# Optimization experiments

Hardware: AMD Instinct MI355X
Metric: run time of the kernel (lower is better)

## Reference

```python
import jax, jax.numpy as jnp
import numpy as np
from jax import lax

B, T, D, H, L = 128, 512, 256, 256, 2


def setup_inputs() -> dict:
    key = jax.random.key(0)
    ks = jax.random.split(key, 8)
    s = 1.0 / np.sqrt(H)
    return {
        "input1": jax.random.normal(ks[0], (B, T, D), jnp.float32),
        "input2": jax.random.normal(ks[1], (B, T, D), jnp.float32),
        "W_ih": jax.random.normal(ks[2], (L, 4 * H, D), jnp.float32) * s,
        "W_hh": jax.random.normal(ks[3], (L, 4 * H, H), jnp.float32) * s,
        "b_ih": jax.random.normal(ks[4], (L, 4 * H), jnp.float32) * s,
        "b_hh": jax.random.normal(ks[5], (L, 4 * H), jnp.float32) * s,
        "fc_w": jax.random.normal(ks[6], (5, H), jnp.float32) * s,
        "fc_b": jax.random.normal(ks[7], (5,), jnp.float32) * s,
    }


def _lstm_layer(x, Wih, Whh, bih, bhh):
    # x: [B, T, in]; returns (outputs [B, T, H], final h [B, H])
    b = x.shape[0]
    # precompute input projection for all timesteps (one big GEMM)
    xg = jnp.einsum('bti,gi->btg', x, Wih) + bih + bhh  # [B, T, 4H]
    h0 = jnp.zeros((b, H), x.dtype)
    c0 = jnp.zeros((b, H), x.dtype)

    def step(carry, xg_t):
        h, c = carry
        gates = xg_t + h @ Whh.T  # [B, 4H]
        i, f, g, o = jnp.split(gates, 4, axis=-1)
        i = jax.nn.sigmoid(i)
        f = jax.nn.sigmoid(f)
        g = jnp.tanh(g)
        o = jax.nn.sigmoid(o)
        c = f * c + i * g
        h = o * jnp.tanh(c)
        return (h, c), h

    (h_last, _), hs = lax.scan(step, (h0, c0), jnp.swapaxes(xg, 0, 1))
    return jnp.swapaxes(hs, 0, 1), h_last


def _forward_once(x, W_ih, W_hh, b_ih, b_hh, fc_w, fc_b):
    h_finals = []
    out = x
    for l in range(L):
        out, h_last = _lstm_layer(out, W_ih[l], W_hh[l], b_ih[l], b_hh[l])
        h_finals.append(h_last)
    hn = jnp.stack(h_finals, axis=0).reshape(-1, H)  # [L*B, H] (torch hn.view)
    return jax.nn.relu(hn) @ fc_w.T + fc_b  # [L*B, 5]


def reference(input1, input2, W_ih, W_hh, b_ih, b_hh, fc_w, fc_b):
    out1 = _forward_once(input1, W_ih, W_hh, b_ih, b_hh, fc_w, fc_b)
    out2 = _forward_once(input2, W_ih, W_hh, b_ih, b_hh, fc_w, fc_b)
    return (out1, out2)
```

## Files before the change

### kernel.cpp

```cpp
#include <hip/hip_runtime.h>
#include <hip/hip_fp16.h>

typedef unsigned int  u32;
typedef unsigned short u16;

typedef _Float16 h2v __attribute__((ext_vector_type(2)));
typedef _Float16 h8v __attribute__((ext_vector_type(8)));
typedef float    f4v __attribute__((ext_vector_type(4)));

static __device__ __forceinline__ u16 f2h_bits(float x){
    _Float16 h = (_Float16)x;
    return __builtin_bit_cast(u16, h);
}
static __device__ __forceinline__ u32 pack2(float a, float b){
    return (u32)f2h_bits(a) | ((u32)f2h_bits(b) << 16);
}
static __device__ __forceinline__ float fdot2(u32 w, u32 h, float acc){
#if __has_builtin(__builtin_amdgcn_fdot2)
    return __builtin_amdgcn_fdot2(__builtin_bit_cast(h2v, w),
                                  __builtin_bit_cast(h2v, h), acc, false);
#else
    h2v wv = __builtin_bit_cast(h2v, w), hv = __builtin_bit_cast(h2v, h);
    return acc + (float)wv[0]*(float)hv[0] + (float)wv[1]*(float)hv[1];
#endif
}
template<int CTRL>
static __device__ __forceinline__ float dpp_qp(float x){
#if __has_builtin(__builtin_amdgcn_mov_dpp)
    int r = __builtin_amdgcn_mov_dpp(__builtin_bit_cast(int, x), CTRL, 0xF, 0xF, true);
    return __builtin_bit_cast(float, r);
#else
    return __shfl_xor(x, (CTRL == 0xB1) ? 1 : 2);
#endif
}


__global__ void cvt_weights(const float* __restrict__ Wih,
                            const float* __restrict__ Whh,
                            const float* __restrict__ bih,
                            const float* __restrict__ bhh,
                            u32* __restrict__ wih16u,
                            u32* __restrict__ wreg,
                            u32* __restrict__ wldsg,
                            float* __restrict__ bias){
    u32 e = blockIdx.x * blockDim.x + threadIdx.x;
    {
        float2 v = ((const float2*)Wih)[e];
        wih16u[e] = pack2(v.x, v.y);
    }
    if (e < 196608u){
        u32 l = (e >= 98304u) ? 1u : 0u;
        u32 rem = e - l*98304u;
        u32 pidx = rem >> 10, L = rem & 1023u;
        u32 r = pidx / 24u, p = pidx - r*24u;
        u32 j = L >> 2, q = L & 3u;
        u32 row = r*256u + j;
        u32 P = 32u*q + p;
        float2 v = ((const float2*)Whh)[((size_t)l*1024u + row)*128u + P];
        wreg[e] = pack2(v.x, v.y);
    } else {
        u32 e2 = e - 196608u;
        u32 l = e2 >> 15, rem = e2 & 32767u;
        u32 i2 = rem >> 10, L = rem & 1023u;
        u32 r = i2 >> 3, k = i2 & 7u;
        u32 j = L >> 2, q = L & 3u;
        u32 row = r*256u + j;
        u32 P = 32u*q + 24u + k;
        float2 v = ((const float2*)Whh)[((size_t)l*1024u + row)*128u + P];
        wldsg[e2] = pack2(v.x, v.y);
    }
    if (e < 2048u){
        u32 l = e >> 10, Ls = e & 1023u;
        u32 src = l*1024u + (((Ls & 3u) << 8) | (Ls >> 2));
        bias[e] = bih[src] + bhh[src];
    }
}

__global__ void cvt_chunk(const float* __restrict__ in1,
                          const float* __restrict__ in2,
                          u16* __restrict__ a16,
                          int t0, int lgTc){
    u32 idx = blockIdx.x * blockDim.x + threadIdx.x;
    u32 c4  = idx & 63;
    u32 row = idx >> 6;
    u32 tc   = row & ((1u << lgTc) - 1u);
    u32 beta = row >> lgTc;
    const float* base = (beta < 128u) ? in1 : in2;
    float4 v = *(const float4*)(base + ((size_t)(beta & 127u)*512u + (size_t)(t0 + tc))*256u + c4*4u);
    ((uint2*)a16)[idx] = make_uint2(pack2(v.x, v.y), pack2(v.z, v.w));
}

__global__ __launch_bounds__(256) void proj_gemm(
        const u16*  __restrict__ A16,
        const u16*  __restrict__ Bw,
        u16*        __restrict__ Cout){
    __shared__ u16 Blds[128][264];
    const int tid = threadIdx.x;
    const int m0 = blockIdx.x * 128;
    const int n0 = blockIdx.y * 128;

    {
        const uint4* src = (const uint4*)Bw;
        #pragma unroll
        for (int i = 0; i < 16; i++){
            int idx = i*256 + tid;
            int r = idx >> 5, c4 = idx & 31;
            uint4 v = src[(size_t)(n0 + r)*32 + c4];
            *(uint4*)&Blds[r][c4*8] = v;
        }
    }
    __syncthreads();

    const int l   = tid & 63;
    const int wid = tid >> 6;
    const int wm = (wid >> 1) * 64;
    const int wn = (wid & 1) * 64;
    const int lr = l & 15;
    const int lk = l >> 4;

    f4v acc[4][4] = {};

    const u16* a16p[4];
    #pragma unroll
    for (int f = 0; f < 4; f++)
        a16p[f] = A16 + (size_t)(m0 + wm + f*16 + lr)*256 + lk*8;

    #pragma unroll
    for (int ks = 0; ks < 8; ks++){
        uint4 a_[4], b_[4];
        #pragma unroll
        for (int f = 0; f < 4; f++)
            a_[f] = *(const uint4*)(a16p[f] + ks*32);
        #pragma unroll
        for (int f = 0; f < 4; f++)
            b_[f] = *(const uint4*)&Blds[wn + f*16 + lr][ks*32 + lk*8];
        #pragma unroll
        for (int fm = 0; fm < 4; fm++)
            #pragma unroll
            for (int fn = 0; fn < 4; fn++)
                acc[fm][fn] = __builtin_amdgcn_mfma_f32_16x16x32_f16(
                    __builtin_bit_cast(h8v, a_[fm]),
                    __builtin_bit_cast(h8v, b_[fn]),
                    acc[fm][fn], 0, 0, 0);
    }

    #pragma unroll
    for (int fm = 0; fm < 4; fm++){
        #pragma unroll
        for (int i = 0; i < 4; i++){
            int m = m0 + wm + fm*16 + lk*4 + i;
            size_t rowoff = (size_t)m*1024;
            #pragma unroll
            for (int fn = 0; fn < 4; fn++){
                int n = n0 + wn + fn*16 + lr;
                int np = ((n & 255) << 2) | (n >> 8);
                Cout[rowoff + np] = f2h_bits(acc[fm][fn][i]);
            }
        }
    }
}

__global__ __launch_bounds__(1024, 4) void lstm_rec(
        const u16* __restrict__ xg,
        const u32* __restrict__ wreg,
        const u32* __restrict__ wldsg,
        const float* __restrict__ bias,
        u16* __restrict__ hseq,
        u16* __restrict__ h_state,
        float* __restrict__ c_state,
        int Tc, int write_seq, int first){
    __shared__ u32 wlds[1024*36];
    __shared__ alignas(16) u16 hbufF[2*288];

    const int L    = threadIdx.x;
    const int q    = L & 3;
    const int j    = L >> 2;
    const int beta = blockIdx.x;

    u32 w[96];
    #pragma unroll
    for (int t = 0; t < 96; t++)
        w[t] = wreg[(size_t)t*1024 + L];
    #pragma unroll
    for (int i = 0; i < 32; i++)
        wlds[L*36 + i] = wldsg[(size_t)i*1024 + L];

    const float bs = bias[L];
    float c = 0.f;
    u16 hb_last = 0;
    if (q == 0){
        u16 h0 = first ? (u16)0 : h_state[(size_t)beta*256 + j];
        hbufF[72*(j >> 6) + (j & 63)] = h0;
        hb_last = h0;
        if (!first) c = c_state[(size_t)beta*256 + j];
    }
    __syncthreads();

    const u16* xr = xg + (size_t)beta * Tc * 1024 + L;
    u16 xcur = xr[0];
    const uint4* wr = (const uint4*)&wlds[L*36];

    for (int tc = 0; tc < Tc; tc++){
        u16 xnext = (tc + 1 < Tc) ? xr[(size_t)(tc+1)*1024] : (u16)0;

        const uint4* hv = (const uint4*)&hbufF[(tc & 1)*288 + 72*q];
        float pA = 0.f, pB = 0.f, pC = 0.f, pD = 0.f;

        #pragma unroll
        for (int i = 0; i < 6; i++){
            uint4 hh = hv[i];
            pA = fdot2(w[   4*i+0], hh.x, pA); pA = fdot2(w[   4*i+1], hh.y, pA);
            pA = fdot2(w[   4*i+2], hh.z, pA); pA = fdot2(w[   4*i+3], hh.w, pA);
            pB = fdot2(w[24+4*i+0], hh.x, pB); pB = fdot2(w[24+4*i+1], hh.y, pB);
            pB = fdot2(w[24+4*i+2], hh.z, pB); pB = fdot2(w[24+4*i+3], hh.w, pB);
            pC = fdot2(w[48+4*i+0], hh.x, pC); pC = fdot2(w[48+4*i+1], hh.y, pC);
            pC = fdot2(w[48+4*i+2], hh.z, pC); pC = fdot2(w[48+4*i+3], hh.w, pC);
            pD = fdot2(w[72+4*i+0], hh.x, pD); pD = fdot2(w[72+4*i+1], hh.y, pD);
            pD = fdot2(w[72+4*i+2], hh.z, pD); pD = fdot2(w[72+4*i+3], hh.w, pD);
        }
        #pragma unroll
        for (int m = 0; m < 2; m++){
            uint4 hh = hv[6+m];
            uint4 wa = wr[0+m], wb = wr[2+m], wc = wr[4+m], wd = wr[6+m];
            pA = fdot2(wa.x, hh.x, pA); pA = fdot2(wa.y, hh.y, pA);
            pA = fdot2(wa.z, hh.z, pA); pA = fdot2(wa.w, hh.w, pA);
            pB = fdot2(wb.x, hh.x, pB); pB = fdot2(wb.y, hh.y, pB);
            pB = fdot2(wb.z, hh.z, pB); pB = fdot2(wb.w, hh.w, pB);
            pC = fdot2(wc.x, hh.x, pC); pC = fdot2(wc.y, hh.y, pC);
            pC = fdot2(wc.z, hh.z, pC); pC = fdot2(wc.w, hh.w, pC);
            pD = fdot2(wd.x, hh.x, pD); pD = fdot2(wd.y, hh.y, pD);
            pD = fdot2(wd.z, hh.z, pD); pD = fdot2(wd.w, hh.w, pD);
        }

        float k0_ = (q & 1) ? pB : pA;
        float k1_ = (q & 1) ? pD : pC;
        float s0_ = (q & 1) ? pA : pB;
        float s1_ = (q & 1) ? pC : pD;
        k0_ += dpp_qp<0xB1>(s0_);
        k1_ += dpp_qp<0xB1>(s1_);
        float kf = (q & 2) ? k1_ : k0_;
        float sf = (q & 2) ? k0_ : k1_;
        kf += dpp_qp<0x4E>(sf);

        float acc = kf + bs + (float)__builtin_bit_cast(_Float16, xcur);

        float targ = (q == 2) ? 2.f*acc : -acc;
        float e1 = __expf(targ);
        float rr = 1.f / (1.f + e1);
        float a  = (q == 2) ? 1.f - 2.f*rr : rr;

        float p1 = dpp_qp<0xB1>(a);
        float p2 = dpp_qp<0x4E>(a);
        float p3 = dpp_qp<0x4E>(p1);

        c = (q == 0) ? (p1*c + a*p2) : 0.f;
        float e2 = __expf(2.f*c);
        float th = 1.f - 2.f/(e2 + 1.f);
        float h  = p3 * th;
        u16 hb = f2h_bits(h);

        if (q == 0){
            hbufF[((tc & 1)^1)*288 + 72*(j >> 6) + (j & 63)] = hb;
            hb_last = hb;
            if (write_seq) hseq[((size_t)beta*Tc + tc)*256 + j] = hb;
        }
        xcur = xnext;
        __syncthreads();
    }

    if (q == 0){
        h_state[(size_t)beta*256 + j] = hb_last;
        c_state[(size_t)beta*256 + j] = c;
    }
}

__global__ void fc_out(const u16* __restrict__ hlast,
                       const float* __restrict__ fcw,
                       const float* __restrict__ fcb,
                       float* __restrict__ out){
    int r = blockIdx.x;
    int lane = threadIdx.x;
    int inp = r >> 8, rem = r & 255, l = rem >> 7, b = rem & 127;
    int beta = inp*128 + b;
    const u16* h = hlast + ((size_t)l*256 + beta)*256;

    int j0 = lane * 4;
    uint2 hb = *(const uint2*)(h + j0);
    h2v p0 = __builtin_bit_cast(h2v, hb.x), p1 = __builtin_bit_cast(h2v, hb.y);
    float hv0 = fmaxf((float)p0[0], 0.f);
    float hv1 = fmaxf((float)p0[1], 0.f);
    float hv2 = fmaxf((float)p1[0], 0.f);
    float hv3 = fmaxf((float)p1[1], 0.f);

    float acc[5];
    #pragma unroll
    for (int k = 0; k < 5; k++){
        float4 w = *(const float4*)(fcw + k*256 + j0);
        acc[k] = hv0*w.x + hv1*w.y + hv2*w.z + hv3*w.w;
    }
    #pragma unroll
    for (int k = 0; k < 5; k++)
        #pragma unroll
        for (int off = 32; off > 0; off >>= 1)
            acc[k] += __shfl_xor(acc[k], off);
    if (lane == 0){
        #pragma unroll
        for (int k = 0; k < 5; k++)
            out[(size_t)r*5 + k] = acc[k] + fcb[k];
    }
}

extern "C" void kernel_launch(void* const* d_in, const int* in_sizes, int n_in,
                              void* d_out, int out_size, void* d_ws, size_t ws_size,
                              hipStream_t stream) {
    const float* in1 = (const float*)d_in[0];
    const float* in2 = (const float*)d_in[1];
    const float* Wih = (const float*)d_in[2];
    const float* Whh = (const float*)d_in[3];
    const float* bih = (const float*)d_in[4];
    const float* bhh = (const float*)d_in[5];
    const float* fcw = (const float*)d_in[6];
    const float* fcb = (const float*)d_in[7];
    float* out = (float*)d_out;

    char* ws = (char*)d_ws;
    u16*   wih16   = (u16*)  (ws + 0x000000);
    u32*   wreg    = (u32*)  (ws + 0x100000);
    u32*   wldsg   = (u32*)  (ws + 0x1C0000);
    float* bias    = (float*)(ws + 0x200000);
    u16*   h_state = (u16*)  (ws + 0x202000);
    float* c_state = (float*)(ws + 0x242000);
    const size_t chunk_off = 0x300000;

    int Tc = 8;
    for (int cand = 512; cand >= 8; cand >>= 1){
        if (chunk_off + (size_t)cand * 655360ull <= ws_size){ Tc = cand; break; }
    }
    int lgTc = 31 - __builtin_clz((u32)Tc);
    u16* xgc = (u16*)(ws + chunk_off);
    u16* hsc = (u16*)(ws + chunk_off + (size_t)Tc * 524288ull);

    cvt_weights<<<1024, 256, 0, stream>>>(Wih, Whh, bih, bhh,
                                          (u32*)wih16, wreg, wldsg, bias);

    const int nch = 512 / Tc;
    dim3 pg(2*Tc, 8);
    for (int k = 0; k < nch; k++){
        int t0 = k * Tc;
        cvt_chunk<<<64*Tc, 256, 0, stream>>>(in1, in2, hsc, t0, lgTc);
        proj_gemm<<<pg, 256, 0, stream>>>(hsc, wih16, xgc);
        lstm_rec<<<256, 1024, 0, stream>>>((const u16*)xgc, wreg, wldsg, bias,
                                           hsc, h_state, c_state,
                                           Tc, 1, k == 0);
        proj_gemm<<<pg, 256, 0, stream>>>(hsc, wih16 + 262144, xgc);
        lstm_rec<<<256, 1024, 0, stream>>>((const u16*)xgc, wreg + 98304, wldsg + 32768,
                                           bias + 1024,
                                           (u16*)nullptr, h_state + 65536, c_state + 65536,
                                           Tc, 0, k == 0);
    }
    fc_out<<<512, 64, 0, stream>>>(h_state, fcw, fcb, out);
}
```

Measured before the change: 2.376 ms.

## Compute LSTM recurrent matvec with MFMA instead of packed fdot2

Replaces the per-thread fdot2 recurrent kernel with an MFMA-based kernel of 512 threads. W_hh is pre-swizzled into MFMA B-fragment layout, with six k-fragments per wave kept in registers and the rest in LDS. h is broadcast as the A operand and only row 0 of each MFMA output is used. The input-gate projection is double-buffered through LDS, and the bias add moves into the projection GEMM epilogue. The aim is to cut the serial per-timestep cost, but the MFMA wastes 15 of 16 output rows and register pressure is high.

```diff
diff --git a/kernel.cpp b/kernel.cpp
--- a/kernel.cpp
+++ b/kernel.cpp
@@ -15,14 +15,8 @@
 static __device__ __forceinline__ u32 pack2(float a, float b){
     return (u32)f2h_bits(a) | ((u32)f2h_bits(b) << 16);
 }
-static __device__ __forceinline__ float fdot2(u32 w, u32 h, float acc){
-#if __has_builtin(__builtin_amdgcn_fdot2)
-    return __builtin_amdgcn_fdot2(__builtin_bit_cast(h2v, w),
-                                  __builtin_bit_cast(h2v, h), acc, false);
-#else
-    h2v wv = __builtin_bit_cast(h2v, w), hv = __builtin_bit_cast(h2v, h);
-    return acc + (float)wv[0]*(float)hv[0] + (float)wv[1]*(float)hv[1];
-#endif
+static __device__ __forceinline__ float h2f(u16 b){
+    return (float)__builtin_bit_cast(_Float16, b);
 }
 template<int CTRL>
 static __device__ __forceinline__ float dpp_qp(float x){
@@ -40,39 +34,27 @@
                             const float* __restrict__ bih,
                             const float* __restrict__ bhh,
                             u32* __restrict__ wih16u,
-                            u32* __restrict__ wreg,
-                            u32* __restrict__ wldsg,
-                            float* __restrict__ bias){
+                            u32* __restrict__ wmf32,
+                            float* __restrict__ biasP){
     u32 e = blockIdx.x * blockDim.x + threadIdx.x;
     {
         float2 v = ((const float2*)Wih)[e];
         wih16u[e] = pack2(v.x, v.y);
     }
-    if (e < 196608u){
-        u32 l = (e >= 98304u) ? 1u : 0u;
-        u32 rem = e - l*98304u;
-        u32 pidx = rem >> 10, L = rem & 1023u;
-        u32 r = pidx / 24u, p = pidx - r*24u;
-        u32 j = L >> 2, q = L & 3u;
-        u32 row = r*256u + j;
-        u32 P = 32u*q + p;
-        float2 v = ((const float2*)Whh)[((size_t)l*1024u + row)*128u + P];
-        wreg[e] = pack2(v.x, v.y);
-    } else {
-        u32 e2 = e - 196608u;
-        u32 l = e2 >> 15, rem = e2 & 32767u;
-        u32 i2 = rem >> 10, L = rem & 1023u;
-        u32 r = i2 >> 3, k = i2 & 7u;
-        u32 j = L >> 2, q = L & 3u;
-        u32 row = r*256u + j;
-        u32 P = 32u*q + 24u + k;
-        float2 v = ((const float2*)Whh)[((size_t)l*1024u + row)*128u + P];
-        wldsg[e2] = pack2(v.x, v.y);
+    {
+        u32 l = e >> 17, rem = e & 131071u;
+        u32 w = rem >> 14, nf = (rem >> 11) & 7u, kf = (rem >> 8) & 7u;
+        u32 lane = (rem >> 2) & 63u, word = rem & 3u;
+        u32 s = w*128u + nf*16u + (lane & 15u);
+        u32 r = (s & 3u)*256u + (s >> 2);
+        u32 k = kf*32u + (lane >> 4)*8u + word*2u;
+        float2 v = ((const float2*)Whh)[((size_t)(l*1024u + r))*128u + (k >> 1)];
+        wmf32[e] = pack2(v.x, v.y);
     }
     if (e < 2048u){
         u32 l = e >> 10, Ls = e & 1023u;
         u32 src = l*1024u + (((Ls & 3u) << 8) | (Ls >> 2));
-        bias[e] = bih[src] + bhh[src];
+        biasP[e] = bih[src] + bhh[src];
     }
 }
 
@@ -93,6 +75,7 @@
 __global__ __launch_bounds__(256) void proj_gemm(
         const u16*  __restrict__ A16,
         const u16*  __restrict__ Bw,
+        const float* __restrict__ biasP,
         u16*        __restrict__ Cout){
     __shared__ u16 Blds[128][264];
     const int tid = threadIdx.x;
@@ -144,6 +127,13 @@
                     acc[fm][fn], 0, 0, 0);
     }
 
+    int np_[4]; float bv_[4];
+    #pragma unroll
+    for (int fn = 0; fn < 4; fn++){
+        int n = n0 + wn + fn*16 + lr;
+        np_[fn] = ((n & 255) << 2) | (n >> 8);
+        bv_[fn] = biasP[np_[fn]];
+    }
     #pragma unroll
     for (int fm = 0; fm < 4; fm++){
         #pragma unroll
@@ -151,126 +141,120 @@
             int m = m0 + wm + fm*16 + lk*4 + i;
             size_t rowoff = (size_t)m*1024;
             #pragma unroll
-            for (int fn = 0; fn < 4; fn++){
-                int n = n0 + wn + fn*16 + lr;
-                int np = ((n & 255) << 2) | (n >> 8);
-                Cout[rowoff + np] = f2h_bits(acc[fm][fn][i]);
-            }
-        }
-    }
-}
-
-__global__ __launch_bounds__(1024, 4) void lstm_rec(
+            for (int fn = 0; fn < 4; fn++)
+                Cout[rowoff + np_[fn]] = f2h_bits(acc[fm][fn][i] + bv_[fn]);
+        }
+    }
+}
+
+__global__ __launch_bounds__(512, 2) void mfma_rec(
         const u16* __restrict__ xg,
-        const u32* __restrict__ wreg,
-        const u32* __restrict__ wldsg,
-        const float* __restrict__ bias,
+        const uint4* __restrict__ wmf,
         u16* __restrict__ hseq,
         u16* __restrict__ h_state,
         float* __restrict__ c_state,
         int Tc, int write_seq, int first){
-    __shared__ u32 wlds[1024*36];
-    __shared__ alignas(16) u16 hbufF[2*288];
-
-    const int L    = threadIdx.x;
-    const int q    = L & 3;
-    const int j    = L >> 2;
+    __shared__ uint4 blds[8192];
+    __shared__ alignas(16) u16 hbuf[2][256];
+    __shared__ alignas(16) u16 xbuf[2][1024];
+
+    const int tid = threadIdx.x;
+    const int w  = tid >> 6, l = tid & 63;
+    const int lr = l & 15,  lk = l >> 4;
+    const int q  = lr & 3;
     const int beta = blockIdx.x;
 
-    u32 w[96];
-    #pragma unroll
-    for (int t = 0; t < 96; t++)
-        w[t] = wreg[(size_t)t*1024 + L];
-    #pragma unroll
-    for (int i = 0; i < 32; i++)
-        wlds[L*36 + i] = wldsg[(size_t)i*1024 + L];
-
-    const float bs = bias[L];
-    float c = 0.f;
-    u16 hb_last = 0;
-    if (q == 0){
-        u16 h0 = first ? (u16)0 : h_state[(size_t)beta*256 + j];
-        hbufF[72*(j >> 6) + (j & 63)] = h0;
-        hb_last = h0;
-        if (!first) c = c_state[(size_t)beta*256 + j];
-    }
+    uint4 wB[8][6];
+    #pragma unroll
+    for (int nf = 0; nf < 8; nf++)
+        #pragma unroll
+        for (int kf = 0; kf < 6; kf++)
+            wB[nf][kf] = wmf[((w*8+nf)*8 + kf)*64 + l];
+    #pragma unroll
+    for (int i = 0; i < 16; i++){
+        int d = i*512 + tid;
+        int lane = d & 63, frag = d >> 6;
+        int kfi = frag & 1, nff = (frag >> 1) & 7, ww = frag >> 4;
+        blds[d] = wmf[((ww*8+nff)*8 + 6+kfi)*64 + lane];
+    }
+
+    float cc[8];
+    #pragma unroll
+    for (int nf = 0; nf < 8; nf++){
+        int j = (w*8+nf)*4 + (lr >> 2);
+        cc[nf] = first ? 0.f : c_state[(size_t)beta*256 + j];
+    }
+    if (tid < 32){
+        uint4 hv = first ? make_uint4(0,0,0,0)
+                         : *(const uint4*)(h_state + (size_t)beta*256 + tid*8);
+        *(uint4*)&hbuf[0][tid*8] = hv;
+    }
+    const u16* xgb = xg + ((size_t)beta * Tc) * 1024;
+    if (tid < 128)
+        *(uint4*)&xbuf[0][tid*8] = *(const uint4*)(xgb + tid*8);
     __syncthreads();
 
-    const u16* xr = xg + (size_t)beta * Tc * 1024 + L;
-    u16 xcur = xr[0];
-    const uint4* wr = (const uint4*)&wlds[L*36];
-
     for (int tc = 0; tc < Tc; tc++){
-        u16 xnext = (tc + 1 < Tc) ? xr[(size_t)(tc+1)*1024] : (u16)0;
-
-        const uint4* hv = (const uint4*)&hbufF[(tc & 1)*288 + 72*q];
-        float pA = 0.f, pB = 0.f, pC = 0.f, pD = 0.f;
-
-        #pragma unroll
-        for (int i = 0; i < 6; i++){
-            uint4 hh = hv[i];
-            pA = fdot2(w[   4*i+0], hh.x, pA); pA = fdot2(w[   4*i+1], hh.y, pA);
-            pA = fdot2(w[   4*i+2], hh.z, pA); pA = fdot2(w[   4*i+3], hh.w, pA);
-            pB = fdot2(w[24+4*i+0], hh.x, pB); pB = fdot2(w[24+4*i+1], hh.y, pB);
-            pB = fdot2(w[24+4*i+2], hh.z, pB); pB = fdot2(w[24+4*i+3], hh.w, pB);
-            pC = fdot2(w[48+4*i+0], hh.x, pC); pC = fdot2(w[48+4*i+1], hh.y, pC);
-            pC = fdot2(w[48+4*i+2], hh.z, pC); pC = fdot2(w[48+4*i+3], hh.w, pC);
-            pD = fdot2(w[72+4*i+0], hh.x, pD); pD = fdot2(w[72+4*i+1], hh.y, pD);
-            pD = fdot2(w[72+4*i+2], hh.z, pD); pD = fdot2(w[72+4*i+3], hh.w, pD);
-        }
-        #pragma unroll
-        for (int m = 0; m < 2; m++){
-            uint4 hh = hv[6+m];
-            uint4 wa = wr[0+m], wb = wr[2+m], wc = wr[4+m], wd = wr[6+m];
-            pA = fdot2(wa.x, hh.x, pA); pA = fdot2(wa.y, hh.y, pA);
-            pA = fdot2(wa.z, hh.z, pA); pA = fdot2(wa.w, hh.w, pA);
-            pB = fdot2(wb.x, hh.x, pB); pB = fdot2(wb.y, hh.y, pB);
-            pB = fdot2(wb.z, hh.z, pB); pB = fdot2(wb.w, hh.w, pB);
-            pC = fdot2(wc.x, hh.x, pC); pC = fdot2(wc.y, hh.y, pC);
-            pC = fdot2(wc.z, hh.z, pC); pC = fdot2(wc.w, hh.w, pC);
-            pD = fdot2(wd.x, hh.x, pD); pD = fdot2(wd.y, hh.y, pD);
-            pD = fdot2(wd.z, hh.z, pD); pD = fdot2(wd.w, hh.w, pD);
-        }
-
-        float k0_ = (q & 1) ? pB : pA;
-        float k1_ = (q & 1) ? pD : pC;
-        float s0_ = (q & 1) ? pA : pB;
-        float s1_ = (q & 1) ? pC : pD;
-        k0_ += dpp_qp<0xB1>(s0_);
-        k1_ += dpp_qp<0xB1>(s1_);
-        float kf = (q & 2) ? k1_ : k0_;
-        float sf = (q & 2) ? k0_ : k1_;
-        kf += dpp_qp<0x4E>(sf);
-
-        float acc = kf + bs + (float)__builtin_bit_cast(_Float16, xcur);
-
-        float targ = (q == 2) ? 2.f*acc : -acc;
-        float e1 = __expf(targ);
-        float rr = 1.f / (1.f + e1);
-        float a  = (q == 2) ? 1.f - 2.f*rr : rr;
-
-        float p1 = dpp_qp<0xB1>(a);
-        float p2 = dpp_qp<0x4E>(a);
-        float p3 = dpp_qp<0x4E>(p1);
-
-        c = (q == 0) ? (p1*c + a*p2) : 0.f;
-        float e2 = __expf(2.f*c);
-        float th = 1.f - 2.f/(e2 + 1.f);
-        float h  = p3 * th;
-        u16 hb = f2h_bits(h);
-
-        if (q == 0){
-            hbufF[((tc & 1)^1)*288 + 72*(j >> 6) + (j & 63)] = hb;
-            hb_last = hb;
-            if (write_seq) hseq[((size_t)beta*Tc + tc)*256 + j] = hb;
-        }
-        xcur = xnext;
+        const int cur = tc & 1, nxt = cur ^ 1;
+
+        if (tid < 128){
+            int stc = (tc + 1 < Tc) ? tc + 1 : tc;
+            *(uint4*)&xbuf[nxt][tid*8] =
+                *(const uint4*)(xgb + (size_t)stc*1024 + tid*8);
+        }
+
+        #pragma unroll
+        for (int pass = 0; pass < 2; pass++){
+            f4v acc[4] = {};
+            #pragma unroll
+            for (int kf = 0; kf < 8; kf++){
+                uint4 av = *(const uint4*)&hbuf[cur][kf*32 + lk*8];
+                #pragma unroll
+                for (int f = 0; f < 4; f++){
+                    const int nf = pass*4 + f;
+                    uint4 bv = (kf < 6) ? wB[nf][kf]
+                                        : blds[((w*8+nf)*2 + (kf-6))*64 + l];
+                    acc[f] = __builtin_amdgcn_mfma_f32_16x16x32_f16(
+                        __builtin_bit_cast(h8v, av),
+                        __builtin_bit_cast(h8v, bv),
+                        acc[f], 0, 0, 0);
+                }
+            }
+            #pragma unroll
+            for (int f = 0; f < 4; f++){
+                const int nf = pass*4 + f;
+                float val = acc[f][0] + h2f(xbuf[cur][w*128 + nf*16 + lr]);
+                float targ = (q == 2) ? 2.f*val : -val;
+                float e1 = __expf(targ);
+                float rr = 1.f / (1.f + e1);
+                float a  = (q == 2) ? 1.f - 2.f*rr : rr;
+                float p1 = dpp_qp<0xB1>(a);
+                float p2 = dpp_qp<0x4E>(a);
+                float p3 = dpp_qp<0x4E>(p1);
+                float cn = p1*cc[nf] + a*p2;
+                cc[nf] = cn;
+                float e2 = __expf(2.f*cn);
+                float th = 1.f - 2.f/(e2 + 1.f);
+                float h  = p3 * th;
+                if ((l & 51) == 0)
+                    hbuf[nxt][(w*8+nf)*4 + (l >> 2)] = f2h_bits(h);
+            }
+        }
         __syncthreads();
-    }
-
-    if (q == 0){
-        h_state[(size_t)beta*256 + j] = hb_last;
-        c_state[(size_t)beta*256 + j] = c;
+
+        if (write_seq && tid < 32){
+            uint4 hv = *(const uint4*)&hbuf[nxt][tid*8];
+            *(uint4*)(hseq + ((size_t)beta*Tc + tc)*256 + tid*8) = hv;
+        }
+    }
+
+    if (tid < 32)
+        *(uint4*)(h_state + (size_t)beta*256 + tid*8) =
+            *(const uint4*)&hbuf[Tc & 1][tid*8];
+    if ((l & 51) == 0){
+        #pragma unroll
+        for (int nf = 0; nf < 8; nf++)
+            c_state[(size_t)beta*256 + (w*8+nf)*4 + (l >> 2)] = cc[nf];
     }
 }
 
@@ -325,9 +309,8 @@
 
     char* ws = (char*)d_ws;
     u16*   wih16   = (u16*)  (ws + 0x000000);
-    u32*   wreg    = (u32*)  (ws + 0x100000);
-    u32*   wldsg   = (u32*)  (ws + 0x1C0000);
-    float* bias    = (float*)(ws + 0x200000);
+    u32*   wmf32   = (u32*)  (ws + 0x100000);
+    float* biasP   = (float*)(ws + 0x200000);
     u16*   h_state = (u16*)  (ws + 0x202000);
     float* c_state = (float*)(ws + 0x242000);
     const size_t chunk_off = 0x300000;
@@ -341,22 +324,22 @@
     u16* hsc = (u16*)(ws + chunk_off + (size_t)Tc * 524288ull);
 
     cvt_weights<<<1024, 256, 0, stream>>>(Wih, Whh, bih, bhh,
-                                          (u32*)wih16, wreg, wldsg, bias);
+                                          (u32*)wih16, wmf32, biasP);
 
     const int nch = 512 / Tc;
     dim3 pg(2*Tc, 8);
+    const uint4* wmf = (const uint4*)wmf32;
     for (int k = 0; k < nch; k++){
         int t0 = k * Tc;
         cvt_chunk<<<64*Tc, 256, 0, stream>>>(in1, in2, hsc, t0, lgTc);
-        proj_gemm<<<pg, 256, 0, stream>>>(hsc, wih16, xgc);
-        lstm_rec<<<256, 1024, 0, stream>>>((const u16*)xgc, wreg, wldsg, bias,
-                                           hsc, h_state, c_state,
-                                           Tc, 1, k == 0);
-        proj_gemm<<<pg, 256, 0, stream>>>(hsc, wih16 + 262144, xgc);
-        lstm_rec<<<256, 1024, 0, stream>>>((const u16*)xgc, wreg + 98304, wldsg + 32768,
-                                           bias + 1024,
-                                           (u16*)nullptr, h_state + 65536, c_state + 65536,
-                                           Tc, 0, k == 0);
+        proj_gemm<<<pg, 256, 0, stream>>>(hsc, wih16, biasP, xgc);
+        mfma_rec<<<256, 512, 0, stream>>>((const u16*)xgc, wmf,
+                                          hsc, h_state, c_state,
+                                          Tc, 1, k == 0);
+        proj_gemm<<<pg, 256, 0, stream>>>(hsc, wih16 + 262144, biasP + 1024, xgc);
+        mfma_rec<<<256, 512, 0, stream>>>((const u16*)xgc, wmf + 32768,
+                                          (u16*)nullptr, h_state + 65536, c_state + 65536,
+                                          Tc, 0, k == 0);
     }
     fc_out<<<512, 64, 0, stream>>>(h_state, fcw, fcb, out);
 }
```

Measured after the change: 3.481 ms. 46.5% more time.
